# Kernel tuning notes

Measured on AMD Instinct MI355X. Metric: run time of the kernel, lower is better.

Reference implementation:

```python
import jax, jax.numpy as jnp
import numpy as np

K = 3
STRIDE = 1
PAD = 1
GROUPS = 16
EPS = 1e-5


def _conv2d(x, w, b, stride, pad):
    out = jax.lax.conv_general_dilated(
        x, w, (stride, stride), [(pad, pad), (pad, pad)],
        dimension_numbers=("NCHW", "OIHW", "NCHW"))
    return out + b[None, :, None, None]


def setup_inputs() -> dict:
    key = jax.random.key(0)
    ks = jax.random.split(key, 6)
    B, Cin, H, W = 4, 256, 64, 64
    Cout = 256
    x = jax.random.normal(ks[0], (B, Cin, H, W), dtype=jnp.float32)
    # DCNv2 offset/mask-generating conv: 3*K*K = 27 output channels
    w_off = jax.random.normal(ks[1], (3 * K * K, Cin, K, K), dtype=jnp.float32) * 0.01
    b_off = jnp.zeros((3 * K * K,), dtype=jnp.float32)
    # main deformable conv weight/bias
    weight = jax.random.normal(ks[2], (Cout, Cin, K, K), dtype=jnp.float32) * 0.02
    bias = jnp.zeros((Cout,), dtype=jnp.float32)
    # GroupNorm affine params
    gamma = jnp.ones((Cout,), dtype=jnp.float32)
    beta = jnp.zeros((Cout,), dtype=jnp.float32)
    return {"x": x, "w_off": w_off, "b_off": b_off,
            "weight": weight, "bias": bias, "gamma": gamma, "beta": beta}


def reference(x, w_off, b_off, weight, bias, gamma, beta):
    B, Cin, H, W = x.shape
    Cout = weight.shape[0]
    KK = K * K

    # --- offset/mask branch (DCNv2): 18 offsets + 9 sigmoid masks ---
    om = _conv2d(x, w_off, b_off, STRIDE, PAD)          # [B, 27, Ho, Wo]
    Ho, Wo = om.shape[2], om.shape[3]
    off_y, off_x, m = jnp.split(om, 3, axis=1)          # each [B, 9, Ho, Wo]
    mask = jax.nn.sigmoid(m)

    # --- sampling coordinates: base grid + kernel tap + learned offset ---
    kgy = jnp.repeat(jnp.arange(K, dtype=x.dtype), K)   # [9] row of tap
    kgx = jnp.tile(jnp.arange(K, dtype=x.dtype), K)     # [9] col of tap
    base_y = jnp.arange(Ho, dtype=x.dtype) * STRIDE - PAD
    base_x = jnp.arange(Wo, dtype=x.dtype) * STRIDE - PAD
    py = base_y[None, None, :, None] + kgy[None, :, None, None] + off_y  # [B,9,Ho,Wo]
    px = base_x[None, None, None, :] + kgx[None, :, None, None] + off_x  # [B,9,Ho,Wo]

    # --- bilinear sampling with zero padding outside the image ---
    y0 = jnp.floor(py)
    x0 = jnp.floor(px)
    wy1 = py - y0
    wx1 = px - x0

    def gather(img, yy, xx):
        # img [Cin,H,W], yy/xx [9,Ho,Wo] int -> [Cin,9,Ho,Wo]
        return img[:, yy, xx]

    def corner(yi, xi, wy, wx):
        valid = (yi >= 0) & (yi < H) & (xi >= 0) & (xi < W)
        yc = jnp.clip(yi, 0, H - 1).astype(jnp.int32)
        xc = jnp.clip(xi, 0, W - 1).astype(jnp.int32)
        vals = jax.vmap(gather)(x, yc, xc)               # [B,Cin,9,Ho,Wo]
        w_ = (wy * wx * valid.astype(x.dtype))[:, None]   # [B,1,9,Ho,Wo]
        return vals * w_

    sampled = (corner(y0, x0, (1 - wy1), (1 - wx1))
               + corner(y0, x0 + 1, (1 - wy1), wx1)
               + corner(y0 + 1, x0, wy1, (1 - wx1))
               + corner(y0 + 1, x0 + 1, wy1, wx1))       # [B,Cin,9,Ho,Wo]
    sampled = sampled * mask[:, None]                     # modulation

    # --- conv accumulation over taps and input channels ---
    out = jnp.einsum("bckhw,ock->bohw", sampled,
                     weight.reshape(Cout, Cin, KK)) + bias[None, :, None, None]

    # --- GroupNorm(16, Cout) ---
    og = out.reshape(B, GROUPS, Cout // GROUPS, Ho, Wo)
    mu = og.mean(axis=(2, 3, 4), keepdims=True)
    var = og.var(axis=(2, 3, 4), keepdims=True)
    og = (og - mu) * jax.lax.rsqrt(var + EPS)
    out = og.reshape(B, Cout, Ho, Wo) * gamma[None, :, None, None] + beta[None, :, None, None]
    return out
```

## Files before the change

### kernel.cpp

```cpp
#include <hip/hip_runtime.h>
#include <math.h>

#define CIN   256
#define COUT  256
#define H     64
#define W     64
#define HW    4096
#define KK    9
#define KC    2304
#define NOFF  27
#define B_    4
#define EPS   1e-5f
#define OM3S  (B_ * NOFF * HW)

typedef __attribute__((ext_vector_type(4))) float f32x4;
typedef __attribute__((ext_vector_type(8))) short s16x8;

static __device__ __forceinline__ unsigned short f2bf(float f) {
  unsigned u = __builtin_bit_cast(unsigned, f);
  u += 0x7FFF + ((u >> 16) & 1);
  return (unsigned short)(u >> 16);
}
static __device__ __forceinline__ float bflo(unsigned u) {
  return __builtin_bit_cast(float, u << 16);
}
static __device__ __forceinline__ float bfhi(unsigned u) {
  return __builtin_bit_cast(float, u & 0xffff0000u);
}
static __device__ __forceinline__ unsigned packbf(float lo, float hi) {
  unsigned ul = __builtin_bit_cast(unsigned, lo);
  unsigned uh = __builtin_bit_cast(unsigned, hi);
  ul += 0x7FFF + ((ul >> 16) & 1);
  uh += 0x7FFF + ((uh >> 16) & 1);
  return (ul >> 16) | (uh & 0xffff0000u);
}

__global__ __launch_bounds__(256) void prep_kernel(
    const float* __restrict__ x, const float* __restrict__ w,
    const float* __restrict__ w_off, unsigned short* __restrict__ xT,
    unsigned short* __restrict__ wBf, unsigned short* __restrict__ wOBf,
    float* __restrict__ gstat) {
  int bi = blockIdx.x;
  int t = threadIdx.x;
  if (bi < 256) {
    __shared__ unsigned short tile[64][272];
    int b = bi >> 6, y = bi & 63;
    const float* src = x + (size_t)b * CIN * HW + y * W;
    for (int r = 0; r < 64; ++r) {
      int idx = r * 256 + t;
      int c = idx >> 6, ww = idx & 63;
      tile[ww][c] = f2bf(src[(size_t)c * HW + ww]);
    }
    __syncthreads();
    unsigned short* dst = xT + ((size_t)(b * 64 + y) * 64) * 256;
    for (int r = 0; r < 8; ++r) {
      int idx = r * 2048 + t * 8;
      int ww = idx >> 8, c = idx & 255;
      *(uint4*)(dst + idx) = *(const uint4*)&tile[ww][c];
    }
  } else if (bi < 544) {
    int pkt = (bi - 256) * 256 + t;
    int lane = pkt & 63;
    int tn = (pkt >> 6) & 15;
    int k2 = pkt >> 10;
    int co = tn * 16 + (lane & 15);
    int kb = k2 * 32 + (lane >> 4) * 8;
    unsigned short v[8];
#pragma unroll
    for (int j = 0; j < 8; ++j) {
      int kk = kb + j;
      int kt = kk >> 8, c = kk & 255;
      v[j] = f2bf(w[(co * 256 + c) * 9 + kt]);
    }
    *(uint4*)&wBf[(size_t)pkt * 8] = *(const uint4*)v;
  } else if (bi < 580) {
    int pkt = (bi - 544) * 256 + t;
    int lane = pkt & 63;
    int tn = (pkt >> 6) & 1;
    int k2 = pkt >> 7;
    int oc = tn * 16 + (lane & 15);
    int kb = k2 * 32 + (lane >> 4) * 8;
    unsigned short v[8];
#pragma unroll
    for (int j = 0; j < 8; ++j) {
      int kk = kb + j;
      int kt = kk >> 8, c = kk & 255;
      v[j] = (oc < NOFF) ? f2bf(w_off[(oc * 256 + c) * 9 + kt]) : (unsigned short)0;
    }
    *(uint4*)&wOBf[(size_t)pkt * 8] = *(const uint4*)v;
  } else {
    if (t < 128) gstat[t] = 0.f;
  }
}

__global__ __launch_bounds__(256) void offconv_mfma_kernel(
    const unsigned short* __restrict__ xT, const unsigned short* __restrict__ wOBf,
    float* __restrict__ om3) {
  int bi = blockIdx.x;
  int ts = bi >> 8;
  int row = bi & 255;
  int b = row >> 6, i = row & 63;
  int t = threadIdx.x, lane = t & 63, wv = t >> 6;
  int lr = lane & 15, lq = lane >> 4;
  int p = wv * 16 + lr;
  const unsigned short* xb = xT + (size_t)b * (HW * 256);
  f32x4 acc[2] = {};

  for (int kc = 0; kc < 3; ++kc) {
    int kt = ts * 3 + kc;
    int ky = kt / 3, kx = kt % 3;
    int yy = i - 1 + ky, xx = p - 1 + kx;
    bool ok = ((unsigned)yy < 64u) && ((unsigned)xx < 64u);
    const unsigned short* ap = xb + ((ok ? yy * 64 + xx : 0) << 8) + lq * 8;
#pragma unroll
    for (int c8 = 0; c8 < 8; ++c8) {
      uint4 av = uint4{0, 0, 0, 0};
      if (ok) av = *(const uint4*)(ap + c8 * 32);
      int k2 = kt * 8 + c8;
      s16x8 a = __builtin_bit_cast(s16x8, av);
      s16x8 b0 = *(const s16x8*)(wOBf + ((((k2 * 2 + 0) << 6) | lane) << 3));
      s16x8 b1 = *(const s16x8*)(wOBf + ((((k2 * 2 + 1) << 6) | lane) << 3));
      acc[0] = __builtin_amdgcn_mfma_f32_16x16x32_bf16(a, b0, acc[0], 0, 0, 0);
      acc[1] = __builtin_amdgcn_mfma_f32_16x16x32_bf16(a, b1, acc[1], 0, 0, 0);
    }
  }
#pragma unroll
  for (int tn = 0; tn < 2; ++tn) {
    int oc = tn * 16 + lr;
    if (oc < NOFF) {
      float* ob = om3 + (size_t)ts * OM3S + ((b * NOFF + oc) << 12) + i * 64 + wv * 16;
#pragma unroll
      for (int r = 0; r < 4; ++r) ob[lq * 4 + r] = acc[tn][r];
    }
  }
}

__global__ __launch_bounds__(256, 2) void gemm_fused_kernel(
    const unsigned short* __restrict__ xT, const float* __restrict__ om3,
    const float* __restrict__ b_off, const unsigned short* __restrict__ wBf,
    const float* __restrict__ bias, unsigned short* __restrict__ cvt,
    float* __restrict__ gstat) {
  __shared__ float tapw[64][KK][4];
  __shared__ int   tapc[64][KK][4];
  __shared__ unsigned short At[2][64 * 64];
  int bi = blockIdx.x;
  int mt = bi & 255;
  int m0 = mt * 64;
  int nh = bi >> 8;
  int b = m0 >> 12;
  int irow = (m0 & 4095) >> 6;
  int t = threadIdx.x, lane = t & 63, wv = t >> 6;
  int lr = lane & 15, lq = lane >> 4;
  const unsigned short* xb = xT + (size_t)b * (HW * 256);

  for (int idx = t; idx < 64 * KK; idx += 256) {
    int p = idx / KK, k = idx % KK;
    int pix = (m0 & 4095) + p;
    size_t o = (size_t)(b * NOFF) * HW + pix;
    float offy = om3[o + k * HW] + om3[OM3S + o + k * HW] +
                 om3[2 * OM3S + o + k * HW] + b_off[k];
    float offx = om3[o + (9 + k) * HW] + om3[OM3S + o + (9 + k) * HW] +
                 om3[2 * OM3S + o + (9 + k) * HW] + b_off[9 + k];
    float mval = om3[o + (18 + k) * HW] + om3[OM3S + o + (18 + k) * HW] +
                 om3[2 * OM3S + o + (18 + k) * HW] + b_off[18 + k];
    float mask = 1.f / (1.f + __expf(-mval));
    float py = (float)(irow - 1 + k / 3) + offy;
    float px = (float)(p - 1 + k % 3) + offx;
    float y0f = floorf(py), x0f = floorf(px);
    float wy1 = py - y0f, wx1 = px - x0f;
    int y0 = (int)y0f, x0 = (int)x0f;
    bool y0ok = (unsigned)y0 < 64u, y1ok = (unsigned)(y0 + 1) < 64u;
    bool x0ok = (unsigned)x0 < 64u, x1ok = (unsigned)(x0 + 1) < 64u;
    tapw[p][k][0] = (1.f - wy1) * (1.f - wx1) * mask * (float)(y0ok && x0ok);
    tapw[p][k][1] = (1.f - wy1) * wx1 * mask * (float)(y0ok && x1ok);
    tapw[p][k][2] = wy1 * (1.f - wx1) * mask * (float)(y1ok && x0ok);
    tapw[p][k][3] = wy1 * wx1 * mask * (float)(y1ok && x1ok);
    int y0c = min(max(y0, 0), 63), y1c = min(max(y0 + 1, 0), 63);
    int x0c = min(max(x0, 0), 63), x1c = min(max(x0 + 1, 0), 63);
    tapc[p][k][0] = (y0c * 64 + x0c) * 256;
    tapc[p][k][1] = (x1c - x0c) * 256;
    tapc[p][k][2] = (y1c - y0c) * 64 * 256;
    tapc[p][k][3] = 0;
  }
  __syncthreads();

  int p = t >> 2, q = t & 3;
  const unsigned short* bb = wBf + ((size_t)((nh * 8 + wv * 2) * 64) + lane) * 8;

  f32x4 acc[4][2] = {};
  s16x8 Bfa[2][2], Bfb[2][2];
  uint4 sG[8];

#define GLOAD(JJ)                                                            \
  {                                                                          \
    int kt_ = (JJ) >> 2, cg_ = (JJ) & 3;                                     \
    int4 tc_ = *(const int4*)&tapc[p][kt_][0];                               \
    const unsigned short* c_ = xb + tc_.x + cg_ * 64 + q * 16;               \
    sG[0] = *(const uint4*)(c_);                                             \
    sG[1] = *(const uint4*)(c_ + 8);                                         \
    sG[2] = *(const uint4*)(c_ + tc_.y);                                     \
    sG[3] = *(const uint4*)(c_ + tc_.y + 8);                                 \
    sG[4] = *(const uint4*)(c_ + tc_.z);                                     \
    sG[5] = *(const uint4*)(c_ + tc_.z + 8);                                 \
    sG[6] = *(const uint4*)(c_ + tc_.z + tc_.y);                             \
    sG[7] = *(const uint4*)(c_ + tc_.z + tc_.y + 8);                         \
  }

#define COMBINE(JJ, BUFI)                                                    \
  {                                                                          \
    int kt_ = (JJ) >> 2;                                                     \
    f32x4 tw_ = *(const f32x4*)&tapw[p][kt_][0];                             \
    _Pragma("unroll") for (int o = 0; o < 2; ++o) {                          \
      const unsigned* a00_ = (const unsigned*)&sG[0 + o];                    \
      const unsigned* a01_ = (const unsigned*)&sG[2 + o];                    \
      const unsigned* a10_ = (const unsigned*)&sG[4 + o];                    \
      const unsigned* a11_ = (const unsigned*)&sG[6 + o];                    \
      uint4 res_;                                                            \
      unsigned* rr_ = (unsigned*)&res_;                                      \
      _Pragma("unroll") for (int u = 0; u < 4; ++u) {                        \
        float lo_ = tw_[0] * bflo(a00_[u]) + tw_[1] * bflo(a01_[u]) +        \
                    tw_[2] * bflo(a10_[u]) + tw_[3] * bflo(a11_[u]);         \
        float hi_ = tw_[0] * bfhi(a00_[u]) + tw_[1] * bfhi(a01_[u]) +        \
                    tw_[2] * bfhi(a10_[u]) + tw_[3] * bfhi(a11_[u]);         \
        rr_[u] = packbf(lo_, hi_);                                           \
      }                                                                      \
      *(uint4*)((char*)At[BUFI] + p * 128 + (((q * 2 + o) ^ (p & 7)) * 16)) = res_; \
    }                                                                        \
  }

#define BISSUE(J, SLOT)                                                      \
  {                                                                          \
    int k2b_ = (J) * 2;                                                      \
    _Pragma("unroll") for (int kh = 0; kh < 2; ++kh)                         \
      _Pragma("unroll") for (int tn = 0; tn < 2; ++tn)                       \
        SLOT[kh][tn] = *(const s16x8*)(bb + (size_t)(k2b_ + kh) * 8192 + tn * 512); \
  }

#define CONSUME(BUFI, SLOT)                                                  \
  {                                                                          \
    const char* buf_ = (const char*)At[BUFI];                                \
    _Pragma("unroll") for (int kh = 0; kh < 2; ++kh) {                       \
      s16x8 af[4];                                                           \
      _Pragma("unroll") for (int tm = 0; tm < 4; ++tm) {                     \
        int r_ = tm * 16 + lr;                                               \
        af[tm] = *(const s16x8*)(buf_ + r_ * 128 + (((kh * 4 + lq) ^ (r_ & 7)) * 16)); \
      }                                                                      \
      __builtin_amdgcn_s_setprio(1);                                         \
      _Pragma("unroll") for (int tm = 0; tm < 4; ++tm)                       \
        _Pragma("unroll") for (int tn = 0; tn < 2; ++tn)                     \
          acc[tm][tn] = __builtin_amdgcn_mfma_f32_16x16x32_bf16(             \
              af[tm], SLOT[kh][tn], acc[tm][tn], 0, 0, 0);                   \
      __builtin_amdgcn_s_setprio(0);                                         \
    }                                                                        \
  }

#define SOFTBAR()                                                            \
  {                                                                          \
    asm volatile("s_waitcnt lgkmcnt(0)" ::: "memory");                       \
    __builtin_amdgcn_sched_barrier(0);                                       \
    __builtin_amdgcn_s_barrier();                                            \
  }

  GLOAD(0);
  COMBINE(0, 0);
  GLOAD(1);
  BISSUE(0, Bfa);
  BISSUE(1, Bfb);
  SOFTBAR();

#pragma unroll 1
  for (int k = 0; k < 36; k += 2) {
    COMBINE(k + 1, 1);
    if (k + 2 < 36) GLOAD(k + 2);
    CONSUME(0, Bfa);
    if (k + 2 < 36) BISSUE(k + 2, Bfa);
    SOFTBAR();
    if (k + 2 < 36) COMBINE(k + 2, 0);
    if (k + 3 < 36) GLOAD(k + 3);
    CONSUME(1, Bfb);
    if (k + 3 < 36) BISSUE(k + 3, Bfb);
    SOFTBAR();
  }

#undef GLOAD
#undef COMBINE
#undef BISSUE
#undef CONSUME
#undef SOFTBAR

  int poff = m0 & 4095;
#pragma unroll
  for (int tn = 0; tn < 2; ++tn) {
    int co = nh * 128 + wv * 32 + tn * 16 + lr;
    float bco = bias[co];
    unsigned short* cvb = cvt + (size_t)(b * COUT + co) * HW + poff;
    float s = 0.f, qq = 0.f;
#pragma unroll
    for (int tm = 0; tm < 4; ++tm) {
      ushort4 st;
#pragma unroll
      for (int r = 0; r < 4; ++r) {
        float v = acc[tm][tn][r] + bco;
        s += v;
        qq += v * v;
        ((unsigned short*)&st)[r] = f2bf(v);
      }
      *(ushort4*)(cvb + tm * 16 + lq * 4) = st;
    }
#pragma unroll
    for (int off = 32; off > 0; off >>= 1) {
      s += __shfl_down(s, off, 64);
      qq += __shfl_down(qq, off, 64);
    }
    if (lane == 0) {
      int g = co >> 4;
      atomicAdd(&gstat[(b * 16 + g) * 2 + 0], s);
      atomicAdd(&gstat[(b * 16 + g) * 2 + 1], qq);
    }
  }
}

__global__ __launch_bounds__(256) void gn_apply_kernel(
    const unsigned short* __restrict__ convout, const float* __restrict__ gstat,
    const float* __restrict__ gamma, const float* __restrict__ beta,
    float* __restrict__ out) {
  int vid = blockIdx.x * 256 + threadIdx.x;
  int e = vid * 8;
  int b = e >> 20;
  int c = (e >> 12) & 255;
  int g = c >> 4;
  float S = gstat[(b * 16 + g) * 2 + 0];
  float Q = gstat[(b * 16 + g) * 2 + 1];
  float mu = S * (1.f / 65536.f);
  float var = Q * (1.f / 65536.f) - mu * mu;
  float rs = rsqrtf(var + EPS);
  float a = rs * gamma[c];
  float bb = beta[c] - mu * a;
  uint4 v = *(const uint4*)(convout + e);
  const unsigned* u = (const unsigned*)&v;
  float4 o0, o1;
  o0.x = bflo(u[0]) * a + bb;  o0.y = bfhi(u[0]) * a + bb;
  o0.z = bflo(u[1]) * a + bb;  o0.w = bfhi(u[1]) * a + bb;
  o1.x = bflo(u[2]) * a + bb;  o1.y = bfhi(u[2]) * a + bb;
  o1.z = bflo(u[3]) * a + bb;  o1.w = bfhi(u[3]) * a + bb;
  *(float4*)(out + e) = o0;
  *(float4*)(out + e + 4) = o1;
}

extern "C" void kernel_launch(void* const* d_in, const int* in_sizes, int n_in,
                              void* d_out, int out_size, void* d_ws, size_t ws_size,
                              hipStream_t stream) {
  const float* x      = (const float*)d_in[0];
  const float* w_off  = (const float*)d_in[1];
  const float* b_off  = (const float*)d_in[2];
  const float* weight = (const float*)d_in[3];
  const float* bias   = (const float*)d_in[4];
  const float* gamma  = (const float*)d_in[5];
  const float* beta   = (const float*)d_in[6];
  float* out = (float*)d_out;

  float* om3 = (float*)d_ws;
  unsigned short* xT   = (unsigned short*)(om3 + (size_t)3 * OM3S);
  unsigned short* wBf  = xT + (size_t)B_ * HW * 256;
  unsigned short* wOBf = wBf + (size_t)COUT * KC;
  unsigned short* cvt  = wOBf + (size_t)32 * KC;
  float* gstat = (float*)(cvt + (size_t)B_ * HW * COUT);

  prep_kernel<<<dim3(581), dim3(256), 0, stream>>>(x, weight, w_off, xT, wBf, wOBf, gstat);
  offconv_mfma_kernel<<<dim3(768), dim3(256), 0, stream>>>(xT, wOBf, om3);
  gemm_fused_kernel<<<dim3(512), dim3(256), 0, stream>>>(xT, om3, b_off, wBf, bias, cvt, gstat);
  gn_apply_kernel<<<dim3(2048), dim3(256), 0, stream>>>(cvt, gstat, gamma, beta, out);
}
```

Before: 176.0 us.

## Halve M tile of fused deformable GEMM to 32 pixels for more occupancy

```diff
diff --git a/kernel.cpp b/kernel.cpp
--- a/kernel.cpp
+++ b/kernel.cpp
@@ -135,25 +135,26 @@
   }
 }
 
-__global__ __launch_bounds__(256, 2) void gemm_fused_kernel(
+__global__ __launch_bounds__(256, 4) void gemm_fused_kernel(
     const unsigned short* __restrict__ xT, const float* __restrict__ om3,
     const float* __restrict__ b_off, const unsigned short* __restrict__ wBf,
     const float* __restrict__ bias, unsigned short* __restrict__ cvt,
     float* __restrict__ gstat) {
-  __shared__ float tapw[64][KK][4];
-  __shared__ int   tapc[64][KK][4];
-  __shared__ unsigned short At[2][64 * 64];
+  __shared__ float tapw[32][KK][4];
+  __shared__ int   tapc[32][KK][4];
+  __shared__ unsigned short At[2][32 * 64];
   int bi = blockIdx.x;
-  int mt = bi & 255;
-  int m0 = mt * 64;
-  int nh = bi >> 8;
+  int mt = bi & 511;
+  int m0 = mt * 32;
+  int nh = bi >> 9;
   int b = m0 >> 12;
   int irow = (m0 & 4095) >> 6;
+  int j0 = m0 & 63;
   int t = threadIdx.x, lane = t & 63, wv = t >> 6;
   int lr = lane & 15, lq = lane >> 4;
   const unsigned short* xb = xT + (size_t)b * (HW * 256);
 
-  for (int idx = t; idx < 64 * KK; idx += 256) {
+  for (int idx = t; idx < 32 * KK; idx += 256) {
     int p = idx / KK, k = idx % KK;
     int pix = (m0 & 4095) + p;
     size_t o = (size_t)(b * NOFF) * HW + pix;
@@ -165,7 +166,7 @@
                  om3[2 * OM3S + o + (18 + k) * HW] + b_off[18 + k];
     float mask = 1.f / (1.f + __expf(-mval));
     float py = (float)(irow - 1 + k / 3) + offy;
-    float px = (float)(p - 1 + k % 3) + offx;
+    float px = (float)(j0 + p - 1 + k % 3) + offx;
     float y0f = floorf(py), x0f = floorf(px);
     float wy1 = py - y0f, wx1 = px - x0f;
     int y0 = (int)y0f, x0 = (int)x0f;
@@ -184,48 +185,42 @@
   }
   __syncthreads();
 
-  int p = t >> 2, q = t & 3;
+  int p = t >> 3, s = t & 7;
   const unsigned short* bb = wBf + ((size_t)((nh * 8 + wv * 2) * 64) + lane) * 8;
 
-  f32x4 acc[4][2] = {};
+  f32x4 acc[2][2] = {};
   s16x8 Bfa[2][2], Bfb[2][2];
-  uint4 sG[8];
+  uint4 sG[4];
 
 #define GLOAD(JJ)                                                            \
   {                                                                          \
     int kt_ = (JJ) >> 2, cg_ = (JJ) & 3;                                     \
     int4 tc_ = *(const int4*)&tapc[p][kt_][0];                               \
-    const unsigned short* c_ = xb + tc_.x + cg_ * 64 + q * 16;               \
+    const unsigned short* c_ = xb + tc_.x + cg_ * 64 + s * 8;                \
     sG[0] = *(const uint4*)(c_);                                             \
-    sG[1] = *(const uint4*)(c_ + 8);                                         \
-    sG[2] = *(const uint4*)(c_ + tc_.y);                                     \
-    sG[3] = *(const uint4*)(c_ + tc_.y + 8);                                 \
-    sG[4] = *(const uint4*)(c_ + tc_.z);                                     \
-    sG[5] = *(const uint4*)(c_ + tc_.z + 8);                                 \
-    sG[6] = *(const uint4*)(c_ + tc_.z + tc_.y);                             \
-    sG[7] = *(const uint4*)(c_ + tc_.z + tc_.y + 8);                         \
+    sG[1] = *(const uint4*)(c_ + tc_.y);                                     \
+    sG[2] = *(const uint4*)(c_ + tc_.z);                                     \
+    sG[3] = *(const uint4*)(c_ + tc_.z + tc_.y);                             \
   }
 
 #define COMBINE(JJ, BUFI)                                                    \
   {                                                                          \
     int kt_ = (JJ) >> 2;                                                     \
     f32x4 tw_ = *(const f32x4*)&tapw[p][kt_][0];                             \
-    _Pragma("unroll") for (int o = 0; o < 2; ++o) {                          \
-      const unsigned* a00_ = (const unsigned*)&sG[0 + o];                    \
-      const unsigned* a01_ = (const unsigned*)&sG[2 + o];                    \
-      const unsigned* a10_ = (const unsigned*)&sG[4 + o];                    \
-      const unsigned* a11_ = (const unsigned*)&sG[6 + o];                    \
-      uint4 res_;                                                            \
-      unsigned* rr_ = (unsigned*)&res_;                                      \
-      _Pragma("unroll") for (int u = 0; u < 4; ++u) {                        \
-        float lo_ = tw_[0] * bflo(a00_[u]) + tw_[1] * bflo(a01_[u]) +        \
-                    tw_[2] * bflo(a10_[u]) + tw_[3] * bflo(a11_[u]);         \
-        float hi_ = tw_[0] * bfhi(a00_[u]) + tw_[1] * bfhi(a01_[u]) +        \
-                    tw_[2] * bfhi(a10_[u]) + tw_[3] * bfhi(a11_[u]);         \
-        rr_[u] = packbf(lo_, hi_);                                           \
-      }                                                                      \
-      *(uint4*)((char*)At[BUFI] + p * 128 + (((q * 2 + o) ^ (p & 7)) * 16)) = res_; \
+    const unsigned* a00_ = (const unsigned*)&sG[0];                          \
+    const unsigned* a01_ = (const unsigned*)&sG[1];                          \
+    const unsigned* a10_ = (const unsigned*)&sG[2];                          \
+    const unsigned* a11_ = (const unsigned*)&sG[3];                          \
+    uint4 res_;                                                              \
+    unsigned* rr_ = (unsigned*)&res_;                                        \
+    _Pragma("unroll") for (int u = 0; u < 4; ++u) {                          \
+      float lo_ = tw_[0] * bflo(a00_[u]) + tw_[1] * bflo(a01_[u]) +          \
+                  tw_[2] * bflo(a10_[u]) + tw_[3] * bflo(a11_[u]);           \
+      float hi_ = tw_[0] * bfhi(a00_[u]) + tw_[1] * bfhi(a01_[u]) +          \
+                  tw_[2] * bfhi(a10_[u]) + tw_[3] * bfhi(a11_[u]);           \
+      rr_[u] = packbf(lo_, hi_);                                             \
     }                                                                        \
+    *(uint4*)((char*)At[BUFI] + p * 128 + (((s ^ (p & 7)) * 16))) = res_;    \
   }
 
 #define BISSUE(J, SLOT)                                                      \
@@ -240,13 +235,13 @@
   {                                                                          \
     const char* buf_ = (const char*)At[BUFI];                                \
     _Pragma("unroll") for (int kh = 0; kh < 2; ++kh) {                       \
-      s16x8 af[4];                                                           \
-      _Pragma("unroll") for (int tm = 0; tm < 4; ++tm) {                     \
+      s16x8 af[2];                                                           \
+      _Pragma("unroll") for (int tm = 0; tm < 2; ++tm) {                     \
         int r_ = tm * 16 + lr;                                               \
         af[tm] = *(const s16x8*)(buf_ + r_ * 128 + (((kh * 4 + lq) ^ (r_ & 7)) * 16)); \
       }                                                                      \
       __builtin_amdgcn_s_setprio(1);                                         \
-      _Pragma("unroll") for (int tm = 0; tm < 4; ++tm)                       \
+      _Pragma("unroll") for (int tm = 0; tm < 2; ++tm)                       \
         _Pragma("unroll") for (int tn = 0; tn < 2; ++tn)                     \
           acc[tm][tn] = __builtin_amdgcn_mfma_f32_16x16x32_bf16(             \
               af[tm], SLOT[kh][tn], acc[tm][tn], 0, 0, 0);                   \
@@ -294,14 +289,14 @@
     int co = nh * 128 + wv * 32 + tn * 16 + lr;
     float bco = bias[co];
     unsigned short* cvb = cvt + (size_t)(b * COUT + co) * HW + poff;
-    float s = 0.f, qq = 0.f;
-#pragma unroll
-    for (int tm = 0; tm < 4; ++tm) {
+    float sS = 0.f, qq = 0.f;
+#pragma unroll
+    for (int tm = 0; tm < 2; ++tm) {
       ushort4 st;
 #pragma unroll
       for (int r = 0; r < 4; ++r) {
         float v = acc[tm][tn][r] + bco;
-        s += v;
+        sS += v;
         qq += v * v;
         ((unsigned short*)&st)[r] = f2bf(v);
       }
@@ -309,12 +304,12 @@
     }
 #pragma unroll
     for (int off = 32; off > 0; off >>= 1) {
-      s += __shfl_down(s, off, 64);
+      sS += __shfl_down(sS, off, 64);
       qq += __shfl_down(qq, off, 64);
     }
     if (lane == 0) {
       int g = co >> 4;
-      atomicAdd(&gstat[(b * 16 + g) * 2 + 0], s);
+      atomicAdd(&gstat[(b * 16 + g) * 2 + 0], sS);
       atomicAdd(&gstat[(b * 16 + g) * 2 + 1], qq);
     }
   }
@@ -368,6 +363,6 @@
 
   prep_kernel<<<dim3(581), dim3(256), 0, stream>>>(x, weight, w_off, xT, wBf, wOBf, gstat);
   offconv_mfma_kernel<<<dim3(768), dim3(256), 0, stream>>>(xT, wOBf, om3);
-  gemm_fused_kernel<<<dim3(512), dim3(256), 0, stream>>>(xT, om3, b_off, wBf, bias, cvt, gstat);
+  gemm_fused_kernel<<<dim3(1024), dim3(256), 0, stream>>>(xT, om3, b_off, wBf, bias, cvt, gstat);
   gn_apply_kernel<<<dim3(2048), dim3(256), 0, stream>>>(cvt, gstat, gamma, beta, out);
 }
```

New measurement: 209.3 us. 19.0% more time.

## Warp-specialize deformable GEMM into producer gather and consumer MFMA waves

Applied to the files above, without the earlier changes.

```diff
diff --git a/kernel.cpp b/kernel.cpp
--- a/kernel.cpp
+++ b/kernel.cpp
@@ -135,7 +135,7 @@
   }
 }
 
-__global__ __launch_bounds__(256, 2) void gemm_fused_kernel(
+__global__ __launch_bounds__(512, 2) void gemm_fused_kernel(
     const unsigned short* __restrict__ xT, const float* __restrict__ om3,
     const float* __restrict__ b_off, const unsigned short* __restrict__ wBf,
     const float* __restrict__ bias, unsigned short* __restrict__ cvt,
@@ -143,17 +143,16 @@
   __shared__ float tapw[64][KK][4];
   __shared__ int   tapc[64][KK][4];
   __shared__ unsigned short At[2][64 * 64];
-  int bi = blockIdx.x;
-  int mt = bi & 255;
+  int mt = blockIdx.x;
   int m0 = mt * 64;
-  int nh = bi >> 8;
   int b = m0 >> 12;
   int irow = (m0 & 4095) >> 6;
-  int t = threadIdx.x, lane = t & 63, wv = t >> 6;
+  int t = threadIdx.x;
+  int lane = t & 63, wv = t >> 6;
   int lr = lane & 15, lq = lane >> 4;
   const unsigned short* xb = xT + (size_t)b * (HW * 256);
 
-  for (int idx = t; idx < 64 * KK; idx += 256) {
+  for (int idx = t; idx < 64 * KK; idx += 512) {
     int p = idx / KK, k = idx % KK;
     int pix = (m0 & 4095) + p;
     size_t o = (size_t)(b * NOFF) * HW + pix;
@@ -184,11 +183,13 @@
   }
   __syncthreads();
 
-  int p = t >> 2, q = t & 3;
-  const unsigned short* bb = wBf + ((size_t)((nh * 8 + wv * 2) * 64) + lane) * 8;
-
-  f32x4 acc[4][2] = {};
-  s16x8 Bfa[2][2], Bfb[2][2];
+  bool isProd = (wv < 4);
+  int p = (t & 255) >> 2, q = t & 3;
+  int cw = isProd ? 0 : (wv - 4);
+  const unsigned short* bb = wBf + ((size_t)(cw * 4) * 64 + lane) * 8;
+
+  f32x4 acc[4][4] = {};
+  s16x8 Bfa[2][4], Bfb[2][4];
   uint4 sG[8];
 
 #define GLOAD(JJ)                                                            \
@@ -232,7 +233,7 @@
   {                                                                          \
     int k2b_ = (J) * 2;                                                      \
     _Pragma("unroll") for (int kh = 0; kh < 2; ++kh)                         \
-      _Pragma("unroll") for (int tn = 0; tn < 2; ++tn)                       \
+      _Pragma("unroll") for (int tn = 0; tn < 4; ++tn)                       \
         SLOT[kh][tn] = *(const s16x8*)(bb + (size_t)(k2b_ + kh) * 8192 + tn * 512); \
   }
 
@@ -247,7 +248,7 @@
       }                                                                      \
       __builtin_amdgcn_s_setprio(1);                                         \
       _Pragma("unroll") for (int tm = 0; tm < 4; ++tm)                       \
-        _Pragma("unroll") for (int tn = 0; tn < 2; ++tn)                     \
+        _Pragma("unroll") for (int tn = 0; tn < 4; ++tn)                     \
           acc[tm][tn] = __builtin_amdgcn_mfma_f32_16x16x32_bf16(             \
               af[tm], SLOT[kh][tn], acc[tm][tn], 0, 0, 0);                   \
       __builtin_amdgcn_s_setprio(0);                                         \
@@ -261,24 +262,33 @@
     __builtin_amdgcn_s_barrier();                                            \
   }
 
-  GLOAD(0);
-  COMBINE(0, 0);
-  GLOAD(1);
-  BISSUE(0, Bfa);
-  BISSUE(1, Bfb);
+  if (isProd) {
+    GLOAD(0);
+    COMBINE(0, 0);
+    GLOAD(1);
+  } else {
+    BISSUE(0, Bfa);
+    BISSUE(1, Bfb);
+  }
   SOFTBAR();
 
 #pragma unroll 1
   for (int k = 0; k < 36; k += 2) {
-    COMBINE(k + 1, 1);
-    if (k + 2 < 36) GLOAD(k + 2);
-    CONSUME(0, Bfa);
-    if (k + 2 < 36) BISSUE(k + 2, Bfa);
+    if (isProd) {
+      COMBINE(k + 1, 1);
+      if (k + 2 < 36) GLOAD(k + 2);
+    } else {
+      CONSUME(0, Bfa);
+      if (k + 2 < 36) BISSUE(k + 2, Bfa);
+    }
     SOFTBAR();
-    if (k + 2 < 36) COMBINE(k + 2, 0);
-    if (k + 3 < 36) GLOAD(k + 3);
-    CONSUME(1, Bfb);
-    if (k + 3 < 36) BISSUE(k + 3, Bfb);
+    if (isProd) {
+      if (k + 2 < 36) COMBINE(k + 2, 0);
+      if (k + 3 < 36) GLOAD(k + 3);
+    } else {
+      CONSUME(1, Bfb);
+      if (k + 3 < 36) BISSUE(k + 3, Bfb);
+    }
     SOFTBAR();
   }
 
@@ -288,34 +298,36 @@
 #undef CONSUME
 #undef SOFTBAR
 
-  int poff = m0 & 4095;
-#pragma unroll
-  for (int tn = 0; tn < 2; ++tn) {
-    int co = nh * 128 + wv * 32 + tn * 16 + lr;
-    float bco = bias[co];
-    unsigned short* cvb = cvt + (size_t)(b * COUT + co) * HW + poff;
-    float s = 0.f, qq = 0.f;
-#pragma unroll
-    for (int tm = 0; tm < 4; ++tm) {
-      ushort4 st;
-#pragma unroll
-      for (int r = 0; r < 4; ++r) {
-        float v = acc[tm][tn][r] + bco;
-        s += v;
-        qq += v * v;
-        ((unsigned short*)&st)[r] = f2bf(v);
+  if (!isProd) {
+    int poff = m0 & 4095;
+#pragma unroll
+    for (int tn = 0; tn < 4; ++tn) {
+      int co = cw * 64 + tn * 16 + lr;
+      float bco = bias[co];
+      unsigned short* cvb = cvt + (size_t)(b * COUT + co) * HW + poff;
+      float sS = 0.f, qq = 0.f;
+#pragma unroll
+      for (int tm = 0; tm < 4; ++tm) {
+        ushort4 st;
+#pragma unroll
+        for (int r = 0; r < 4; ++r) {
+          float v = acc[tm][tn][r] + bco;
+          sS += v;
+          qq += v * v;
+          ((unsigned short*)&st)[r] = f2bf(v);
+        }
+        *(ushort4*)(cvb + tm * 16 + lq * 4) = st;
       }
-      *(ushort4*)(cvb + tm * 16 + lq * 4) = st;
-    }
-#pragma unroll
-    for (int off = 32; off > 0; off >>= 1) {
-      s += __shfl_down(s, off, 64);
-      qq += __shfl_down(qq, off, 64);
-    }
-    if (lane == 0) {
-      int g = co >> 4;
-      atomicAdd(&gstat[(b * 16 + g) * 2 + 0], s);
-      atomicAdd(&gstat[(b * 16 + g) * 2 + 1], qq);
+#pragma unroll
+      for (int off = 32; off > 0; off >>= 1) {
+        sS += __shfl_down(sS, off, 64);
+        qq += __shfl_down(qq, off, 64);
+      }
+      if (lane == 0) {
+        int g = co >> 4;
+        atomicAdd(&gstat[(b * 16 + g) * 2 + 0], sS);
+        atomicAdd(&gstat[(b * 16 + g) * 2 + 1], qq);
+      }
     }
   }
 }
@@ -368,6 +380,6 @@
 
   prep_kernel<<<dim3(581), dim3(256), 0, stream>>>(x, weight, w_off, xT, wBf, wOBf, gstat);
   offconv_mfma_kernel<<<dim3(768), dim3(256), 0, stream>>>(xT, wOBf, om3);
-  gemm_fused_kernel<<<dim3(512), dim3(256), 0, stream>>>(xT, om3, b_off, wBf, bias, cvt, gstat);
+  gemm_fused_kernel<<<dim3(256), dim3(512), 0, stream>>>(xT, om3, b_off, wBf, bias, cvt, gstat);
   gn_apply_kernel<<<dim3(2048), dim3(256), 0, stream>>>(cvt, gstat, gamma, beta, out);
 }
```

Result: faster. 164.5 us (-6.5%).
